# Kernel optimization log

Hardware: AMD Instinct MI355X
Metric: run time of the kernel (lower is better)

## Reference

```python
import jax, jax.numpy as jnp
import numpy as np

B, T, D, U = 32, 4096, 256, 256


def setup_inputs() -> dict:
    key = jax.random.key(0)
    ks = jax.random.split(key, 5)
    s = 1.0 / np.sqrt(D)
    return {
        "query": jax.random.normal(ks[0], (B, D), jnp.float32),
        "values": jax.random.normal(ks[1], (B, T, D), jnp.float32),
        "W1": jax.random.normal(ks[2], (D, U), jnp.float32) * s,
        "b1": jnp.zeros((U,), jnp.float32),
        "W2": jax.random.normal(ks[3], (D, U), jnp.float32) * s,
        "b2": jnp.zeros((U,), jnp.float32),
        "V": jax.random.normal(ks[4], (U, 1), jnp.float32) * (1.0 / np.sqrt(U)),
        "bV": jnp.zeros((1,), jnp.float32),
    }


def reference(query, values, W1, b1, W2, b2, V, bV):
    # score[b,t,u] = tanh(values @ W1 + b1 + (query @ W2 + b2)[:,None,:])
    proj_v = jnp.einsum("btd,du->btu", values, W1) + b1        # [B,T,U]
    proj_q = (query @ W2 + b2)[:, None, :]                      # [B,1,U]
    score = jnp.tanh(proj_v + proj_q) @ V + bV                  # [B,T,1]
    attn = jax.nn.softmax(score, axis=1)                        # softmax over T
    context = jnp.sum(attn * values, axis=1)                    # [B,D]
    return (context, attn)
```

## Files before the change

### kernel.cpp

```cpp
#include <hip/hip_runtime.h>
#include <hip/hip_bf16.h>

typedef __attribute__((ext_vector_type(4))) float f32x4;
typedef __attribute__((ext_vector_type(8))) short s16x8;
typedef __attribute__((ext_vector_type(4))) short s16x4;

static constexpr int Bn = 32;
static constexpr int Tn = 4096;
static constexpr int Dn = 256;
static constexpr int Un = 256;
static constexpr int NBLK = 16;

__device__ __forceinline__ ushort f2bf(float f) {
    unsigned x = __float_as_uint(f);
    x += 0x7fffu + ((x >> 16) & 1u);
    return (ushort)(x >> 16);
}
__device__ __forceinline__ float bf2f(ushort u) {
    return __uint_as_float(((unsigned)u) << 16);
}

__device__ __forceinline__ float fast_tanh(float x) {
    float ax = fabsf(x);
    float e = __expf(-2.0f * ax);
    float r = __fdividef(1.0f - e, 1.0f + e);
    return copysignf(r, x);
}

__global__ __launch_bounds__(256) void k_prep(const float* __restrict__ W1,
                                              ushort* __restrict__ W1T,
                                              const float* __restrict__ query,
                                              const float* __restrict__ W2,
                                              const float* __restrict__ b1,
                                              const float* __restrict__ b2,
                                              float* __restrict__ qb) {
    __shared__ float qs[Dn];
    if (blockIdx.x < 256) {
        const int u = blockIdx.x, d = threadIdx.x;
        W1T[u * Dn + d] = f2bf(W1[d * Un + u]);
    } else {
        const int b = blockIdx.x - 256, u = threadIdx.x;
        qs[u] = query[b * Dn + u];
        __syncthreads();
        float acc = b1[u] + b2[u];
        #pragma unroll 8
        for (int d = 0; d < Dn; ++d) acc += qs[d] * W2[d * Un + u];
        qb[b * Un + u] = acc;
    }
}

__global__ __launch_bounds__(256, 2) void k_fused(const float* __restrict__ values,
                                                  const ushort* __restrict__ W1T,
                                                  const float* __restrict__ qb,
                                                  const float* __restrict__ Vw,
                                                  const float* __restrict__ bV,
                                                  float* __restrict__ scores,
                                                  float* __restrict__ pM,
                                                  float* __restrict__ pS,
                                                  float* __restrict__ pctx) {
    __shared__ __align__(16) ushort Bl[2][32][264];
    __shared__ float sred[4][32];
    __shared__ float slp[32];
    __shared__ float sfac[2];
    __shared__ float runMS[2];
    __shared__ f32x4 cred[4][64];

    const int tid = threadIdx.x;
    const int b = blockIdx.y, blk = blockIdx.x;
    const int wid = tid >> 6, lane = tid & 63;
    const int l15 = lane & 15, hi = lane >> 4;
    const int d4 = (tid & 63) * 4, tg = tid >> 6;

    const float* vbase = values + ((size_t)b * Tn + blk * 256) * Dn;
    const ushort* wbase = W1T + (size_t)(wid * 64 + l15) * Dn + hi * 8;

    float Vreg[4], qreg[4];
    #pragma unroll
    for (int ut = 0; ut < 4; ++ut) {
        int u = wid * 64 + ut * 16 + l15;
        Vreg[ut] = Vw[u];
        qreg[ut] = qb[b * Un + u];
    }
    const float bv = bV[0];

    if (tid == 0) { runMS[0] = -1e30f; runMS[1] = 0.f; }

    f32x4 stg[8];
    #pragma unroll
    for (int i = 0; i < 8; ++i) {
        int idx = i * 256 + tid;
        stg[i] = *(const f32x4*)&vbase[(idx >> 6) * Dn + (idx & 63) * 4];
    }

    f32x4 cacc = (f32x4){0.f, 0.f, 0.f, 0.f};

    #pragma unroll 1
    for (int ck = 0; ck < 8; ++ck) {
        const int cur = ck & 1;

        #pragma unroll
        for (int i = 0; i < 8; ++i) {
            int idx = i * 256 + tid;
            s16x4 p;
            p[0] = (short)f2bf(stg[i][0]); p[1] = (short)f2bf(stg[i][1]);
            p[2] = (short)f2bf(stg[i][2]); p[3] = (short)f2bf(stg[i][3]);
            *(s16x4*)&Bl[cur][idx >> 6][(idx & 63) * 4] = p;
        }
        __syncthreads();

        if (ck < 7) {
            const float* vb = vbase + (ck + 1) * 32 * Dn;
            #pragma unroll
            for (int i = 0; i < 8; ++i) {
                int idx = i * 256 + tid;
                stg[i] = *(const f32x4*)&vb[(idx >> 6) * Dn + (idx & 63) * 4];
            }
        }

        s16x8 bfn0[4], bfn1[4];
        #pragma unroll
        for (int ut = 0; ut < 4; ++ut)
            bfn0[ut] = *(const s16x8*)&wbase[(size_t)ut * 16 * Dn];
        #pragma unroll
        for (int ut = 0; ut < 4; ++ut)
            bfn1[ut] = *(const s16x8*)&wbase[(size_t)ut * 16 * Dn + 32];

        f32x4 acc[2][4];
        #pragma unroll
        for (int tt = 0; tt < 2; ++tt)
            #pragma unroll
            for (int ut = 0; ut < 4; ++ut) acc[tt][ut] = (f32x4){0.f, 0.f, 0.f, 0.f};

        #pragma unroll
        for (int kc = 0; kc < 8; ++kc) {
            s16x8 bf[4];
            #pragma unroll
            for (int ut = 0; ut < 4; ++ut) { bf[ut] = bfn0[ut]; bfn0[ut] = bfn1[ut]; }
            if (kc < 6) {
                #pragma unroll
                for (int ut = 0; ut < 4; ++ut)
                    bfn1[ut] = *(const s16x8*)&wbase[(size_t)ut * 16 * Dn + (kc + 2) * 32];
            }
            s16x8 af[2];
            #pragma unroll
            for (int tt = 0; tt < 2; ++tt)
                af[tt] = *(const s16x8*)&Bl[cur][tt * 16 + l15][kc * 32 + hi * 8];
            #pragma unroll
            for (int tt = 0; tt < 2; ++tt)
                #pragma unroll
                for (int ut = 0; ut < 4; ++ut)
                    acc[tt][ut] = __builtin_amdgcn_mfma_f32_16x16x32_bf16(af[tt], bf[ut], acc[tt][ut], 0, 0, 0);
        }

        float psc[2][4];
        #pragma unroll
        for (int tt = 0; tt < 2; ++tt)
            #pragma unroll
            for (int i = 0; i < 4; ++i) psc[tt][i] = 0.f;
        #pragma unroll
        for (int tt = 0; tt < 2; ++tt)
            #pragma unroll
            for (int ut = 0; ut < 4; ++ut)
                #pragma unroll
                for (int i = 0; i < 4; ++i)
                    psc[tt][i] += fast_tanh(acc[tt][ut][i] + qreg[ut]) * Vreg[ut];
        #pragma unroll
        for (int tt = 0; tt < 2; ++tt)
            #pragma unroll
            for (int i = 0; i < 4; ++i) {
                float v = psc[tt][i];
                v += __shfl_xor(v, 1, 64);
                v += __shfl_xor(v, 2, 64);
                v += __shfl_xor(v, 4, 64);
                v += __shfl_xor(v, 8, 64);
                if (l15 == 0) sred[wid][tt * 16 + hi * 4 + i] = v;
            }
        __syncthreads();

        if (tid < 64) {
            const int row = lane & 31;
            float s = sred[0][row] + sred[1][row] + sred[2][row] + sred[3][row] + bv;
            if (lane < 32) scores[b * Tn + blk * 256 + ck * 32 + row] = s;
            float m = s;
            #pragma unroll
            for (int off = 16; off > 0; off >>= 1) m = fmaxf(m, __shfl_xor(m, off, 64));
            float p = __expf(s - m);
            float S = p;
            #pragma unroll
            for (int off = 16; off > 0; off >>= 1) S += __shfl_xor(S, off, 64);
            if (lane < 32) slp[row] = p;
            if (lane == 0) {
                float Mold = runMS[0];
                float Mnew = fmaxf(Mold, m);
                float sco = __expf(Mold - Mnew);
                float scc = __expf(m - Mnew);
                sfac[0] = sco; sfac[1] = scc;
                runMS[0] = Mnew;
                runMS[1] = runMS[1] * sco + S * scc;
            }
        }
        __syncthreads();

        const float sco = sfac[0], scc = sfac[1];
        f32x4 loc = (f32x4){0.f, 0.f, 0.f, 0.f};
        #pragma unroll
        for (int t = tg; t < 32; t += 4) {
            const float p = slp[t];
            const s16x4 v = *(const s16x4*)&Bl[cur][t][d4];
            loc[0] += p * bf2f((ushort)v[0]);
            loc[1] += p * bf2f((ushort)v[1]);
            loc[2] += p * bf2f((ushort)v[2]);
            loc[3] += p * bf2f((ushort)v[3]);
        }
        cacc = cacc * sco + loc * scc;
    }

    cred[tg][tid & 63] = cacc;
    __syncthreads();
    if (tg == 0) {
        const f32x4 o = cred[0][tid] + cred[1][tid] + cred[2][tid] + cred[3][tid];
        *(f32x4*)&pctx[((size_t)(b * NBLK + blk)) * Dn + d4] = o;
    }
    if (tid == 0) {
        pM[b * NBLK + blk] = runMS[0];
        pS[b * NBLK + blk] = runMS[1];
    }
}

__global__ __launch_bounds__(256) void k_reduce(const float* __restrict__ pM,
                                                const float* __restrict__ pS,
                                                const float* __restrict__ pctx,
                                                float* __restrict__ context,
                                                float* __restrict__ MS) {
    const int b = blockIdx.x, d = threadIdx.x;
    float M = -1e30f;
    #pragma unroll
    for (int c = 0; c < NBLK; ++c) M = fmaxf(M, pM[b * NBLK + c]);
    float S = 0.f, ctx = 0.f;
    #pragma unroll
    for (int c = 0; c < NBLK; ++c) {
        const float w = __expf(pM[b * NBLK + c] - M);
        S += w * pS[b * NBLK + c];
        ctx += w * pctx[((size_t)(b * NBLK + c)) * Dn + d];
    }
    context[b * Dn + d] = __fdividef(ctx, S);
    if (d == 0) { MS[b * 2] = M; MS[b * 2 + 1] = S; }
}

__global__ __launch_bounds__(256) void k_attn(float* __restrict__ attn,
                                              const float* __restrict__ MS) {
    const int b = blockIdx.y;
    const int base = b * Tn + blockIdx.x * 1024 + threadIdx.x * 4;
    const float M = MS[b * 2];
    const float invS = __fdividef(1.0f, MS[b * 2 + 1]);
    float4 s = *(const float4*)&attn[base];
    s.x = __expf(s.x - M) * invS;
    s.y = __expf(s.y - M) * invS;
    s.z = __expf(s.z - M) * invS;
    s.w = __expf(s.w - M) * invS;
    *(float4*)&attn[base] = s;
}

extern "C" void kernel_launch(void* const* d_in, const int* in_sizes, int n_in,
                              void* d_out, int out_size, void* d_ws, size_t ws_size,
                              hipStream_t stream) {
    const float* query  = (const float*)d_in[0];
    const float* values = (const float*)d_in[1];
    const float* W1     = (const float*)d_in[2];
    const float* b1     = (const float*)d_in[3];
    const float* W2     = (const float*)d_in[4];
    const float* b2     = (const float*)d_in[5];
    const float* Vw     = (const float*)d_in[6];
    const float* bV     = (const float*)d_in[7];

    float* context = (float*)d_out;
    float* attn    = (float*)d_out + Bn * Dn;

    float*  pctx = (float*)d_ws;
    float*  pM   = pctx + (size_t)Bn * NBLK * Dn;
    float*  pS   = pM + Bn * NBLK;
    float*  qb   = pS + Bn * NBLK;
    float*  MS   = qb + Bn * Un;
    ushort* W1T  = (ushort*)(MS + Bn * 2);

    k_prep<<<dim3(256 + Bn), dim3(256), 0, stream>>>(W1, W1T, query, W2, b1, b2, qb);
    k_fused<<<dim3(NBLK, Bn), dim3(256), 0, stream>>>(values, W1T, qb, Vw, bV,
                                                      attn, pM, pS, pctx);
    k_reduce<<<dim3(Bn), dim3(256), 0, stream>>>(pM, pS, pctx, context, MS);
    k_attn<<<dim3(Tn / 1024, Bn), dim3(256), 0, stream>>>(attn, MS);
}
```

Baseline: 77.11 us.

## Stage values tiles via direct global-to-LDS loads in fp32 with XOR swizzle

Replaces register staging plus bf16 conversion before the LDS store with global_load_lds DMA of raw fp32 value rows into a double-buffered, XOR-swizzled LDS tile. The conversion to bf16 now happens at MFMA operand load time using the packed v_cvt_pk_bf16_f32 instruction, and the context accumulation reads full fp32 values. This removes the register staging and VGPR pressure and overlaps the next tile's load with compute. In exchange LDS use doubles (64KB for the fp32 tiles), which may cap occupancy, and each MFMA A-fragment now needs more LDS reads and conversions.

```diff
diff --git a/kernel.cpp b/kernel.cpp
--- a/kernel.cpp
+++ b/kernel.cpp
@@ -3,7 +3,6 @@
 
 typedef __attribute__((ext_vector_type(4))) float f32x4;
 typedef __attribute__((ext_vector_type(8))) short s16x8;
-typedef __attribute__((ext_vector_type(4))) short s16x4;
 
 static constexpr int Bn = 32;
 static constexpr int Tn = 4096;
@@ -16,8 +15,11 @@
     x += 0x7fffu + ((x >> 16) & 1u);
     return (ushort)(x >> 16);
 }
-__device__ __forceinline__ float bf2f(ushort u) {
-    return __uint_as_float(((unsigned)u) << 16);
+
+__device__ __forceinline__ unsigned cvt_pk_bf16(float a, float b) {
+    unsigned r;
+    asm("v_cvt_pk_bf16_f32 %0, %1, %2" : "=v"(r) : "v"(a), "v"(b));
+    return r;
 }
 
 __device__ __forceinline__ float fast_tanh(float x) {
@@ -25,6 +27,12 @@
     float e = __expf(-2.0f * ax);
     float r = __fdividef(1.0f - e, 1.0f + e);
     return copysignf(r, x);
+}
+
+__device__ __forceinline__ void gload_lds16(const void* g, void* l) {
+    __builtin_amdgcn_global_load_lds(
+        (const __attribute__((address_space(1))) unsigned*)g,
+        (__attribute__((address_space(3))) unsigned*)l, 16, 0, 0);
 }
 
 __global__ __launch_bounds__(256) void k_prep(const float* __restrict__ W1,
@@ -58,7 +66,7 @@
                                                   float* __restrict__ pM,
                                                   float* __restrict__ pS,
                                                   float* __restrict__ pctx) {
-    __shared__ __align__(16) ushort Bl[2][32][264];
+    __shared__ __align__(16) float Afl[2][32][256];
     __shared__ float sred[4][32];
     __shared__ float slp[32];
     __shared__ float sfac[2];
@@ -69,7 +77,6 @@
     const int b = blockIdx.y, blk = blockIdx.x;
     const int wid = tid >> 6, lane = tid & 63;
     const int l15 = lane & 15, hi = lane >> 4;
-    const int d4 = (tid & 63) * 4, tg = tid >> 6;
 
     const float* vbase = values + ((size_t)b * Tn + blk * 256) * Dn;
     const ushort* wbase = W1T + (size_t)(wid * 64 + l15) * Dn + hi * 8;
@@ -85,37 +92,26 @@
 
     if (tid == 0) { runMS[0] = -1e30f; runMS[1] = 0.f; }
 
-    f32x4 stg[8];
-    #pragma unroll
-    for (int i = 0; i < 8; ++i) {
-        int idx = i * 256 + tid;
-        stg[i] = *(const f32x4*)&vbase[(idx >> 6) * Dn + (idx & 63) * 4];
-    }
+    auto stage = [&](int ck, int buf) {
+        const float* vc = vbase + (size_t)ck * 32 * Dn;
+        #pragma unroll
+        for (int j = 0; j < 8; ++j) {
+            const int r = wid * 8 + j;
+            const float* src = vc + (size_t)r * Dn + (((lane * 16) ^ ((r & 7) << 4)) >> 2);
+            gload_lds16(src, &Afl[buf][r][0]);
+        }
+    };
+
+    stage(0, 0);
 
     f32x4 cacc = (f32x4){0.f, 0.f, 0.f, 0.f};
 
     #pragma unroll 1
     for (int ck = 0; ck < 8; ++ck) {
         const int cur = ck & 1;
-
-        #pragma unroll
-        for (int i = 0; i < 8; ++i) {
-            int idx = i * 256 + tid;
-            s16x4 p;
-            p[0] = (short)f2bf(stg[i][0]); p[1] = (short)f2bf(stg[i][1]);
-            p[2] = (short)f2bf(stg[i][2]); p[3] = (short)f2bf(stg[i][3]);
-            *(s16x4*)&Bl[cur][idx >> 6][(idx & 63) * 4] = p;
-        }
-        __syncthreads();
-
-        if (ck < 7) {
-            const float* vb = vbase + (ck + 1) * 32 * Dn;
-            #pragma unroll
-            for (int i = 0; i < 8; ++i) {
-                int idx = i * 256 + tid;
-                stg[i] = *(const f32x4*)&vb[(idx >> 6) * Dn + (idx & 63) * 4];
-            }
-        }
+        __syncthreads();
+
+        if (ck < 7) stage(ck + 1, cur ^ 1);
 
         s16x8 bfn0[4], bfn1[4];
         #pragma unroll
@@ -141,15 +137,23 @@
                 for (int ut = 0; ut < 4; ++ut)
                     bfn1[ut] = *(const s16x8*)&wbase[(size_t)ut * 16 * Dn + (kc + 2) * 32];
             }
-            s16x8 af[2];
-            #pragma unroll
-            for (int tt = 0; tt < 2; ++tt)
-                af[tt] = *(const s16x8*)&Bl[cur][tt * 16 + l15][kc * 32 + hi * 8];
-            #pragma unroll
-            for (int tt = 0; tt < 2; ++tt)
+            const int cbyte = kc * 128 + hi * 32;
+            #pragma unroll
+            for (int tt = 0; tt < 2; ++tt) {
+                const int r = tt * 16 + l15;
+                const int xr = (r & 7) << 4;
+                const float* pa = &Afl[cur][r][0];
+                const f32x4 f0 = *(const f32x4*)(pa + ((cbyte ^ xr) >> 2));
+                const f32x4 f1 = *(const f32x4*)(pa + (((cbyte + 16) ^ xr) >> 2));
+                union { s16x8 v; unsigned u[4]; } af;
+                af.u[0] = cvt_pk_bf16(f0[0], f0[1]);
+                af.u[1] = cvt_pk_bf16(f0[2], f0[3]);
+                af.u[2] = cvt_pk_bf16(f1[0], f1[1]);
+                af.u[3] = cvt_pk_bf16(f1[2], f1[3]);
                 #pragma unroll
                 for (int ut = 0; ut < 4; ++ut)
-                    acc[tt][ut] = __builtin_amdgcn_mfma_f32_16x16x32_bf16(af[tt], bf[ut], acc[tt][ut], 0, 0, 0);
+                    acc[tt][ut] = __builtin_amdgcn_mfma_f32_16x16x32_bf16(af.v, bf[ut], acc[tt][ut], 0, 0, 0);
+            }
         }
 
         float psc[2][4];
@@ -202,24 +206,28 @@
         __syncthreads();
 
         const float sco = sfac[0], scc = sfac[1];
+        const int cb = (tid & 63) * 16;
+        const int tg = tid >> 6;
         f32x4 loc = (f32x4){0.f, 0.f, 0.f, 0.f};
         #pragma unroll
         for (int t = tg; t < 32; t += 4) {
             const float p = slp[t];
-            const s16x4 v = *(const s16x4*)&Bl[cur][t][d4];
-            loc[0] += p * bf2f((ushort)v[0]);
-            loc[1] += p * bf2f((ushort)v[1]);
-            loc[2] += p * bf2f((ushort)v[2]);
-            loc[3] += p * bf2f((ushort)v[3]);
+            const float* pr = &Afl[cur][t][0];
+            const f32x4 v = *(const f32x4*)(pr + ((cb ^ ((t & 7) << 4)) >> 2));
+            loc[0] += p * v[0];
+            loc[1] += p * v[1];
+            loc[2] += p * v[2];
+            loc[3] += p * v[3];
         }
         cacc = cacc * sco + loc * scc;
     }
 
+    const int tg = tid >> 6;
     cred[tg][tid & 63] = cacc;
     __syncthreads();
     if (tg == 0) {
         const f32x4 o = cred[0][tid] + cred[1][tid] + cred[2][tid] + cred[3][tid];
-        *(f32x4*)&pctx[((size_t)(b * NBLK + blk)) * Dn + d4] = o;
+        *(f32x4*)&pctx[((size_t)(b * NBLK + blk)) * Dn + (tid & 63) * 4] = o;
     }
     if (tid == 0) {
         pM[b * NBLK + blk] = runMS[0];
```

Measured after the change: 87.89 us. +14.0%, slower.
